# Kernel tuning notes

Measured on AMD Instinct MI355X. Metric: run time of the kernel, lower is better.

## Reference

```python
import jax, jax.numpy as jnp
import numpy as np

B, S, E, H = 4, 4096, 768, 8
D = E // H  # head_dim = 96


def setup_inputs() -> dict:
    key = jax.random.key(0)
    ks = jax.random.split(key, 9)
    std = 1.0 / np.sqrt(E)
    return {
        "values": jax.random.normal(ks[0], (B, S, E), dtype=jnp.float32),
        "keys": jax.random.normal(ks[1], (B, S, E), dtype=jnp.float32),
        "query": jax.random.normal(ks[2], (B, S, E), dtype=jnp.float32),
        "mask": jax.random.randint(ks[3], (B, S, 1, 1), 0, 2, dtype=jnp.int32),
        "Wv": jax.random.normal(ks[4], (E, E), dtype=jnp.float32) * std,
        "Wk": jax.random.normal(ks[5], (E, E), dtype=jnp.float32) * std,
        "Wq": jax.random.normal(ks[6], (E, E), dtype=jnp.float32) * std,
        "Wo": jax.random.normal(ks[7], (E, E), dtype=jnp.float32) * std,
        "bo": jax.random.normal(ks[8], (E,), dtype=jnp.float32) * std,
    }


def reference(values, keys, query, mask, Wv, Wk, Wq, Wo, bo):
    b, s, e = query.shape
    h, d = H, e // H
    scale = e ** 0.5

    def split(x, W):
        # Linear (no bias) then view to [b, s, h, d] and permute to [b, h, s, d]
        return (x @ W.T).reshape(b, s, h, d).transpose(0, 2, 1, 3)

    v = split(values, Wv)   # [b, h, s, d]
    k = split(keys, Wk)     # [b, h, s, d]
    q = split(query, Wq)    # [b, h, s, d]

    # Faithful to torch.einsum('nqhd,nkhd->nhqk', q, k) with q,k laid out as
    # [b, h, s, d]: this contracts over d with s batched, producing a per-token
    # head-gram matrix att[b, s, i, j] = sum_d q[b,i,s,d] * k[b,j,s,d].
    att = jnp.einsum('bisd,bjsd->bsij', q, k)          # [b, s, h, h]
    att = jnp.where(mask == 0, jnp.float32(-1e20), att)
    att = jax.nn.softmax(att / scale, axis=3)

    # torch.einsum('nhql,nlhd->nqhd', att, v) with att [b,s,h,h], v [b,h,s,d]:
    # out[b, i, s, d] = sum_j att[b,s,i,j] * v[b,j,s,d]  -> [b, h, s, d]
    out = jnp.einsum('bsij,bjsd->bisd', att, v)        # [b, h, s, d]
    out = out.reshape(b, s, h * d)                      # row-major, matches torch .reshape
    return out @ Wo.T + bo
```

## Files before the change

kernel.cpp:

```cpp
#include <hip/hip_runtime.h>
#include <hip/hip_bf16.h>
#include <cstdint>


typedef unsigned short u16;
typedef short bf16x8 __attribute__((ext_vector_type(8)));
typedef float f32x4 __attribute__((ext_vector_type(4)));

#define B_  4
#define S_  4096
#define E_  768
#define H_  8
#define D_  96
#define T_  (B_*S_)
#define NT_ (E_/128)
#define KSTEPS_ (E_/64)

static __device__ __forceinline__ u16 f2bf(float f) {
  unsigned u = __builtin_bit_cast(unsigned, f);
  u += 0x7fffu + ((u >> 16) & 1u);
  return (u16)(u >> 16);
}
static __device__ __forceinline__ unsigned pk2(float lo, float hi) {
  return (unsigned)f2bf(lo) | ((unsigned)f2bf(hi) << 16);
}
static __device__ __forceinline__ float bflo(unsigned u) {
  return __builtin_bit_cast(float, u << 16);
}
static __device__ __forceinline__ float bfhi(unsigned u) {
  return __builtin_bit_cast(float, u & 0xffff0000u);
}

__global__ __launch_bounds__(256) void conv_bf16(
    const float* __restrict__ src, u16* __restrict__ dst)
{
  const int i = blockIdx.x * 256 + threadIdx.x;
  const float4 v = ((const float4*)src)[i];
  uint2 w;
  w.x = pk2(v.x, v.y);
  w.y = pk2(v.z, v.w);
  ((uint2*)dst)[i] = w;
}

template<bool OUT_F32, bool BIAS>
__global__ __launch_bounds__(256, 3) void gemm_nt(
    const u16* __restrict__ A, const float* __restrict__ W,
    const float* __restrict__ bias, void* __restrict__ Cv)
{
  __shared__ u16 lA[128 * 64];
  __shared__ u16 lB[128 * 64];
  const int tid  = threadIdx.x;
  const int wave = tid >> 6;
  const int lane = tid & 63;
  const int wr = wave >> 1, wc = wave & 1;
  const int bid = blockIdx.x;
  const int wg  = (bid & 7) * (gridDim.x >> 3) + (bid >> 3);
  const int mT  = wg / NT_;
  const int nT  = wg - mT * NT_;
  const int tM = mT << 7, tN = nT << 7;
  const int l15 = lane & 15, l4 = lane >> 4;

  f32x4 acc[4][4] = {};

  for (int kt = 0; kt < E_; kt += 64) {
    __syncthreads();
#pragma unroll
    for (int c = 0; c < 4; ++c) {
      const int idx = (c << 8) + tid;
      const int r = idx >> 3, g = idx & 7;
      const int gs = g ^ (r & 7);
      const u16* ga = A + (tM + r) * E_ + kt + gs * 8;
      __builtin_amdgcn_global_load_lds(
          (const __attribute__((address_space(1))) void*)ga,
          (__attribute__((address_space(3))) void*)&lA[(((c << 8) + (wave << 6)) << 3)],
          16, 0, 0);
    }
#pragma unroll
    for (int c = 0; c < 4; ++c) {
      const int idx = (c << 8) + tid;
      const int r = idx >> 3, g = idx & 7;
      const float* gw = W + (tN + r) * E_ + kt + g * 8;
      const float4 w0 = *(const float4*)gw;
      const float4 w1 = *(const float4*)(gw + 4);
      uint4 pkd;
      pkd.x = pk2(w0.x, w0.y);
      pkd.y = pk2(w0.z, w0.w);
      pkd.z = pk2(w1.x, w1.y);
      pkd.w = pk2(w1.z, w1.w);
      const int gs = g ^ (r & 7);
      *(uint4*)&lB[r * 64 + gs * 8] = pkd;
    }
    __syncthreads();

#pragma unroll
    for (int kk = 0; kk < 2; ++kk) {
      bf16x8 a[4], b[4];
#pragma unroll
      for (int m = 0; m < 4; ++m) {
        const int rA = wr * 64 + m * 16 + l15;
        const int gA = (kk << 2) + l4;
        a[m] = *(const bf16x8*)&lA[rA * 64 + ((gA ^ (rA & 7)) << 3)];
      }
#pragma unroll
      for (int n = 0; n < 4; ++n) {
        const int rB = wc * 64 + n * 16 + l15;
        const int gB = (kk << 2) + l4;
        b[n] = *(const bf16x8*)&lB[rB * 64 + ((gB ^ (rB & 7)) << 3)];
      }
#pragma unroll
      for (int m = 0; m < 4; ++m)
#pragma unroll
        for (int n = 0; n < 4; ++n)
          acc[m][n] = __builtin_amdgcn_mfma_f32_16x16x32_bf16(a[m], b[n], acc[m][n], 0, 0, 0);
    }
  }

  const int cr = l4 * 4;
#pragma unroll
  for (int m = 0; m < 4; ++m) {
#pragma unroll
    for (int n = 0; n < 4; ++n) {
      const int row = tM + wr * 64 + m * 16 + cr;
      const int col = tN + wc * 64 + n * 16 + l15;
      const float badd = BIAS ? bias[col] : 0.f;
#pragma unroll
      for (int r = 0; r < 4; ++r) {
        const float val = acc[m][n][r] + badd;
        if constexpr (OUT_F32)
          ((float*)Cv)[(size_t)(row + r) * E_ + col] = val;
        else
          ((u16*)Cv)[(size_t)(row + r) * E_ + col] = f2bf(val);
      }
    }
  }
}

__global__ __launch_bounds__(256) void attn_tok(
    const u16* __restrict__ Q, const u16* __restrict__ K,
    const u16* __restrict__ V, const int* __restrict__ mask,
    u16* __restrict__ O)
{
  __shared__ float pl[4][8][8];
  const int tid = threadIdx.x, wave = tid >> 6, lane = tid & 63;
  const int t = blockIdx.x * 4 + wave;
  const int s = t & (S_ - 1);
  const int b = t >> 12;
  const int i = lane >> 3, j = lane & 7;

  const uint4* qp = (const uint4*)(Q + (size_t)t * E_ + i * D_);
  const uint4* kp = (const uint4*)(K + (size_t)t * E_ + j * D_);
  float acc = 0.f;
#pragma unroll
  for (int it = 0; it < 12; ++it) {
    const uint4 qv = qp[it], kv = kp[it];
    acc += bflo(qv.x) * bflo(kv.x) + bfhi(qv.x) * bfhi(kv.x);
    acc += bflo(qv.y) * bflo(kv.y) + bfhi(qv.y) * bfhi(kv.y);
    acc += bflo(qv.z) * bflo(kv.z) + bfhi(qv.z) * bfhi(kv.z);
    acc += bflo(qv.w) * bflo(kv.w) + bfhi(qv.w) * bfhi(kv.w);
  }
  float sv = (mask[t] == 0) ? -1e20f : acc;
  sv *= 0.03608439182435161f;
  float mx = sv;
  mx = fmaxf(mx, __shfl_xor(mx, 1));
  mx = fmaxf(mx, __shfl_xor(mx, 2));
  mx = fmaxf(mx, __shfl_xor(mx, 4));
  const float e = __expf(sv - mx);
  float sm = e;
  sm += __shfl_xor(sm, 1);
  sm += __shfl_xor(sm, 2);
  sm += __shfl_xor(sm, 4);
  pl[wave][i][j] = e / sm;
  __syncthreads();

  const int i2 = lane >> 3, db = lane & 7;
  float o[12] = {};
#pragma unroll
  for (int jj = 0; jj < 8; ++jj) {
    const float pj = pl[wave][i2][jj];
    const uint2* vp = (const uint2*)(V + (size_t)t * E_ + jj * D_ + db * 12);
    const uint2 v0 = vp[0], v1 = vp[1], v2 = vp[2];
    o[0]  += pj * bflo(v0.x);  o[1]  += pj * bfhi(v0.x);
    o[2]  += pj * bflo(v0.y);  o[3]  += pj * bfhi(v0.y);
    o[4]  += pj * bflo(v1.x);  o[5]  += pj * bfhi(v1.x);
    o[6]  += pj * bflo(v1.y);  o[7]  += pj * bfhi(v1.y);
    o[8]  += pj * bflo(v2.x);  o[9]  += pj * bfhi(v2.x);
    o[10] += pj * bflo(v2.y);  o[11] += pj * bfhi(v2.y);
  }
  const size_t row = (size_t)b * S_ + 512 * i2 + (s >> 3);
  u16* op = O + row * E_ + 96 * (s & 7) + db * 12;
  uint2 w0, w1, w2;
  w0.x = pk2(o[0], o[1]);
  w0.y = pk2(o[2], o[3]);
  w1.x = pk2(o[4], o[5]);
  w1.y = pk2(o[6], o[7]);
  w2.x = pk2(o[8], o[9]);
  w2.y = pk2(o[10], o[11]);
  ((uint2*)op)[0] = w0;
  ((uint2*)op)[1] = w1;
  ((uint2*)op)[2] = w2;
}

extern "C" void kernel_launch(void* const* d_in, const int* in_sizes, int n_in,
                              void* d_out, int out_size, void* d_ws, size_t ws_size,
                              hipStream_t stream)
{
  const float* values = (const float*)d_in[0];
  const float* keys   = (const float*)d_in[1];
  const float* query  = (const float*)d_in[2];
  const int*   mask   = (const int*)d_in[3];
  const float* Wv = (const float*)d_in[4];
  const float* Wk = (const float*)d_in[5];
  const float* Wq = (const float*)d_in[6];
  const float* Wo = (const float*)d_in[7];
  const float* bo = (const float*)d_in[8];

  const size_t TE = (size_t)T_ * E_;
  u16* Qb = (u16*)d_ws;
  u16* Kb = Qb + TE;
  u16* Vb = Kb + TE;
  u16* Xt = Vb + TE;

  dim3 blk(256);
  dim3 gg(T_ / 128 * NT_);
  dim3 gc(TE / 4 / 256);

  conv_bf16<<<gc, blk, 0, stream>>>(query, Xt);
  gemm_nt<false, false><<<gg, blk, 0, stream>>>(Xt, Wq, nullptr, Qb);
  conv_bf16<<<gc, blk, 0, stream>>>(keys, Xt);
  gemm_nt<false, false><<<gg, blk, 0, stream>>>(Xt, Wk, nullptr, Kb);
  conv_bf16<<<gc, blk, 0, stream>>>(values, Xt);
  gemm_nt<false, false><<<gg, blk, 0, stream>>>(Xt, Wv, nullptr, Vb);

  attn_tok<<<dim3(T_ / 4), blk, 0, stream>>>(Qb, Kb, Vb, mask, Xt );

  gemm_nt<true, true><<<gg, blk, 0, stream>>>(Xt , Wo, bo, (float*)d_out);
}
```

Measured before the change: 201.3 us.

## Pre-convert weights to bf16 and shrink GEMM N-tile to 64

Adds a single kernel that converts all four weight matrices to bf16 up front, so each GEMM tile loads the B operand with async global-to-LDS copies instead of loading fp32 and converting inline. The GEMM tile also shrinks from 128x128 to 128x64, doubling the grid and raising the occupancy hint from 3 to 6 blocks per CU. This aims to cut redundant weight conversion and bandwidth and to improve latency hiding, at the cost of less A-operand reuse per tile and one extra launch.

```diff
diff --git a/kernel.cpp b/kernel.cpp
--- a/kernel.cpp
+++ b/kernel.cpp
@@ -13,8 +13,9 @@
 #define H_  8
 #define D_  96
 #define T_  (B_*S_)
-#define NT_ (E_/128)
-#define KSTEPS_ (E_/64)
+#define BM_ 128
+#define BN_ 64
+#define NT_ (E_/BN_)
 
 static __device__ __forceinline__ u16 f2bf(float f) {
   unsigned u = __builtin_bit_cast(unsigned, f);
@@ -42,13 +43,29 @@
   ((uint2*)dst)[i] = w;
 }
 
+__global__ __launch_bounds__(256) void conv_w(
+    const float* __restrict__ w0, const float* __restrict__ w1,
+    const float* __restrict__ w2, const float* __restrict__ w3,
+    u16* __restrict__ dst)
+{
+  const int bpw = (E_ * E_ / 4) / 256;
+  const int which = blockIdx.x / bpw;
+  const float* src = which == 0 ? w0 : which == 1 ? w1 : which == 2 ? w2 : w3;
+  const int i = (blockIdx.x - which * bpw) * 256 + threadIdx.x;
+  const float4 v = ((const float4*)src)[i];
+  uint2 w;
+  w.x = pk2(v.x, v.y);
+  w.y = pk2(v.z, v.w);
+  ((uint2*)(dst + (size_t)which * E_ * E_))[i] = w;
+}
+
 template<bool OUT_F32, bool BIAS>
-__global__ __launch_bounds__(256, 3) void gemm_nt(
-    const u16* __restrict__ A, const float* __restrict__ W,
+__global__ __launch_bounds__(256, 6) void gemm_nt(
+    const u16* __restrict__ A, const u16* __restrict__ W,
     const float* __restrict__ bias, void* __restrict__ Cv)
 {
-  __shared__ u16 lA[128 * 64];
-  __shared__ u16 lB[128 * 64];
+  __shared__ u16 lA[BM_ * 64];
+  __shared__ u16 lB[BN_ * 64];
   const int tid  = threadIdx.x;
   const int wave = tid >> 6;
   const int lane = tid & 63;
@@ -57,10 +74,10 @@
   const int wg  = (bid & 7) * (gridDim.x >> 3) + (bid >> 3);
   const int mT  = wg / NT_;
   const int nT  = wg - mT * NT_;
-  const int tM = mT << 7, tN = nT << 7;
+  const int tM = mT * BM_, tN = nT * BN_;
   const int l15 = lane & 15, l4 = lane >> 4;
 
-  f32x4 acc[4][4] = {};
+  f32x4 acc[4][2] = {};
 
   for (int kt = 0; kt < E_; kt += 64) {
     __syncthreads();
@@ -72,29 +89,25 @@
       const u16* ga = A + (tM + r) * E_ + kt + gs * 8;
       __builtin_amdgcn_global_load_lds(
           (const __attribute__((address_space(1))) void*)ga,
-          (__attribute__((address_space(3))) void*)&lA[(((c << 8) + (wave << 6)) << 3)],
+          (__attribute__((address_space(3))) void*)&lA[((c << 8) + (wave << 6)) << 3],
           16, 0, 0);
     }
 #pragma unroll
-    for (int c = 0; c < 4; ++c) {
+    for (int c = 0; c < 2; ++c) {
       const int idx = (c << 8) + tid;
       const int r = idx >> 3, g = idx & 7;
-      const float* gw = W + (tN + r) * E_ + kt + g * 8;
-      const float4 w0 = *(const float4*)gw;
-      const float4 w1 = *(const float4*)(gw + 4);
-      uint4 pkd;
-      pkd.x = pk2(w0.x, w0.y);
-      pkd.y = pk2(w0.z, w0.w);
-      pkd.z = pk2(w1.x, w1.y);
-      pkd.w = pk2(w1.z, w1.w);
       const int gs = g ^ (r & 7);
-      *(uint4*)&lB[r * 64 + gs * 8] = pkd;
+      const u16* gb = W + (tN + r) * E_ + kt + gs * 8;
+      __builtin_amdgcn_global_load_lds(
+          (const __attribute__((address_space(1))) void*)gb,
+          (__attribute__((address_space(3))) void*)&lB[((c << 8) + (wave << 6)) << 3],
+          16, 0, 0);
     }
     __syncthreads();
 
 #pragma unroll
     for (int kk = 0; kk < 2; ++kk) {
-      bf16x8 a[4], b[4];
+      bf16x8 a[4], b[2];
 #pragma unroll
       for (int m = 0; m < 4; ++m) {
         const int rA = wr * 64 + m * 16 + l15;
@@ -102,15 +115,15 @@
         a[m] = *(const bf16x8*)&lA[rA * 64 + ((gA ^ (rA & 7)) << 3)];
       }
 #pragma unroll
-      for (int n = 0; n < 4; ++n) {
-        const int rB = wc * 64 + n * 16 + l15;
+      for (int n = 0; n < 2; ++n) {
+        const int rB = wc * 32 + n * 16 + l15;
         const int gB = (kk << 2) + l4;
         b[n] = *(const bf16x8*)&lB[rB * 64 + ((gB ^ (rB & 7)) << 3)];
       }
 #pragma unroll
       for (int m = 0; m < 4; ++m)
 #pragma unroll
-        for (int n = 0; n < 4; ++n)
+        for (int n = 0; n < 2; ++n)
           acc[m][n] = __builtin_amdgcn_mfma_f32_16x16x32_bf16(a[m], b[n], acc[m][n], 0, 0, 0);
     }
   }
@@ -119,9 +132,9 @@
 #pragma unroll
   for (int m = 0; m < 4; ++m) {
 #pragma unroll
-    for (int n = 0; n < 4; ++n) {
+    for (int n = 0; n < 2; ++n) {
       const int row = tM + wr * 64 + m * 16 + cr;
-      const int col = tN + wc * 64 + n * 16 + l15;
+      const int col = tN + wc * 32 + n * 16 + l15;
       const float badd = BIAS ? bias[col] : 0.f;
 #pragma unroll
       for (int r = 0; r < 4; ++r) {
@@ -215,23 +228,27 @@
   const float* bo = (const float*)d_in[8];
 
   const size_t TE = (size_t)T_ * E_;
+  const size_t EE = (size_t)E_ * E_;
   u16* Qb = (u16*)d_ws;
   u16* Kb = Qb + TE;
   u16* Vb = Kb + TE;
   u16* Xt = Vb + TE;
+  u16* Wb = Xt + TE;
 
   dim3 blk(256);
-  dim3 gg(T_ / 128 * NT_);
+  dim3 gg(T_ / BM_ * NT_);
   dim3 gc(TE / 4 / 256);
 
+  conv_w<<<dim3(4 * (E_ * E_ / 4) / 256), blk, 0, stream>>>(Wq, Wk, Wv, Wo, Wb);
+
   conv_bf16<<<gc, blk, 0, stream>>>(query, Xt);
-  gemm_nt<false, false><<<gg, blk, 0, stream>>>(Xt, Wq, nullptr, Qb);
+  gemm_nt<false, false><<<gg, blk, 0, stream>>>(Xt, Wb + 0 * EE, nullptr, Qb);
   conv_bf16<<<gc, blk, 0, stream>>>(keys, Xt);
-  gemm_nt<false, false><<<gg, blk, 0, stream>>>(Xt, Wk, nullptr, Kb);
+  gemm_nt<false, false><<<gg, blk, 0, stream>>>(Xt, Wb + 1 * EE, nullptr, Kb);
   conv_bf16<<<gc, blk, 0, stream>>>(values, Xt);
-  gemm_nt<false, false><<<gg, blk, 0, stream>>>(Xt, Wv, nullptr, Vb);
+  gemm_nt<false, false><<<gg, blk, 0, stream>>>(Xt, Wb + 2 * EE, nullptr, Vb);
 
   attn_tok<<<dim3(T_ / 4), blk, 0, stream>>>(Qb, Kb, Vb, mask, Xt );
 
-  gemm_nt<true, true><<<gg, blk, 0, stream>>>(Xt , Wo, bo, (float*)d_out);
-}
+  gemm_nt<true, true><<<gg, blk, 0, stream>>>(Xt , Wb + 3 * EE, bo, (float*)d_out);
+}
```

Result: slower. 236.8 us (+17.6%).
